# Kernel tuning notes

Hardware: AMD Instinct MI355X
Metric: run time of the kernel (lower is better)

The kernel has to match this reference:

```python
import jax, jax.numpy as jnp
import numpy as np

# dims: batch, seq_len, d_model, heads, head_dim, n_buckets
B, L, DM, H, DH, K = 4, 4096, 1024, 16, 64, 8
C = L // K            # chunk length after bucket sort (512); extra_len==0 for these dims
CS = 0.1              # cluster_score mixing weight


def setup_inputs() -> dict:
    key = jax.random.key(0)
    ks = jax.random.split(key, 12)
    s = 0.02
    def p(k, shape):
        return jax.random.normal(k, shape, jnp.float32) * s
    return {
        "inputs_q": jax.random.normal(ks[0], (B, L, DM), jnp.float32),
        "wq": p(ks[1], (DM, H, DH)), "bq": jnp.zeros((H, DH), jnp.float32),
        "wk": p(ks[2], (DM, H, DH)), "bk": jnp.zeros((H, DH), jnp.float32),
        "wv": p(ks[3], (DM, H, DH)), "bv": jnp.zeros((H, DH), jnp.float32),
        "w_shared": p(ks[4], (H, DH, K)),
        "w_qscore": p(ks[5], (H, DH, K)),
        "w_kscore": p(ks[6], (H, DH, K)),
        "wo": p(ks[7], (H, DH, DM)), "bo": jnp.zeros((DM,), jnp.float32),
    }


def reference(inputs_q, wq, bq, wk, bk, wv, bv, w_shared, w_qscore, w_kscore, wo, bo):
    scale = 1.0 / np.sqrt(DH)
    # QKV projections (DenseGeneral to (H, DH))
    q = jnp.einsum('bld,dhk->blhk', inputs_q, wq) + bq  # [B,L,H,DH]
    k = jnp.einsum('bld,dhk->blhk', inputs_q, wk) + bk
    v = jnp.einsum('bld,dhk->blhk', inputs_q, wv) + bv

    # learned linear cluster scores on stop-gradient q/k
    mix_q = (1.0 - CS) * w_shared + CS * w_qscore  # [H,DH,K]
    mix_k = (1.0 - CS) * w_shared + CS * w_kscore
    qs = jnp.einsum('blhd,hdk->blhk', jax.lax.stop_gradient(q), mix_q)  # [B,L,H,K]
    ksc = jnp.einsum('blhd,hdk->blhk', jax.lax.stop_gradient(k), mix_k)

    # bucket assignment = argmax learned score; per-(batch,head) stable sort by bucket id
    bq_id = jnp.argmax(qs, -1).transpose(0, 2, 1)   # [B,H,L]
    bk_id = jnp.argmax(ksc, -1).transpose(0, 2, 1)
    sort_q = jnp.argsort(bq_id, axis=-1)            # stable in jax
    sort_k = jnp.argsort(bk_id, axis=-1)

    qh = q.transpose(0, 2, 1, 3)  # [B,H,L,DH]
    kh = k.transpose(0, 2, 1, 3)
    vh = v.transpose(0, 2, 1, 3)
    sq = jnp.take_along_axis(qh, sort_q[..., None], axis=2).reshape(B, H, K, C, DH)
    sk = jnp.take_along_axis(kh, sort_k[..., None], axis=2).reshape(B, H, K, C, DH)
    sv = jnp.take_along_axis(vh, sort_k[..., None], axis=2).reshape(B, H, K, C, DH)

    # block attention within each bucket chunk
    logits = jnp.einsum('bhncd,bhned->bhnce', sq, sk) * scale  # [B,H,K,C,C]
    attn = jax.nn.softmax(logits, axis=-1)
    o = jnp.einsum('bhnce,bhned->bhncd', attn, sv).reshape(B, H, L, DH)

    # unsort back to original token order
    inv_q = jnp.argsort(sort_q, axis=-1)
    o = jnp.take_along_axis(o, inv_q[..., None], axis=2)  # [B,H,L,DH]
    o = o.transpose(0, 2, 1, 3)                            # [B,L,H,DH]

    out = jnp.einsum('blhd,hdo->blo', o, wo) + bo          # output projection

    # auxiliary load-balancing routing loss over buckets (extra_loss)
    p_q = jax.nn.softmax(qs, -1)
    p_k = jax.nn.softmax(ksc, -1)
    f_q = jax.nn.one_hot(jnp.argmax(qs, -1), K, dtype=qs.dtype)
    f_k = jax.nn.one_hot(jnp.argmax(ksc, -1), K, dtype=qs.dtype)
    lq = K * jnp.mean(jnp.sum(jnp.mean(f_q, 1) * jnp.mean(p_q, 1), -1))
    lk = K * jnp.mean(jnp.sum(jnp.mean(f_k, 1) * jnp.mean(p_k, 1), -1))
    extra_loss = 0.5 * (lq + lk)
    return out, extra_loss
```

## Files before the change

kernel.cpp:

```cpp
#include <hip/hip_runtime.h>
#include <hip/hip_bf16.h>

#define BB 4
#define LL 4096
#define DM 1024
#define HH 16
#define DHD 64
#define KB 8
#define BL 16384
#define FLAGCAP 131072

typedef __attribute__((ext_vector_type(8))) short short8;
typedef __attribute__((ext_vector_type(4))) short short4v;
typedef __attribute__((ext_vector_type(4))) float float4v;

#define MFMA16(A, Bx, C) __builtin_amdgcn_mfma_f32_16x16x32_bf16(A, Bx, C, 0, 0, 0)

static __device__ __forceinline__ short bf16s(float f) {
  __hip_bfloat16 h = __float2bfloat16(f);
  return *reinterpret_cast<short*>(&h);
}
static __device__ __forceinline__ float b2f(short s) {
  __hip_bfloat16 h = *reinterpret_cast<__hip_bfloat16*>(&s);
  return __bfloat162float(h);
}
static __device__ __forceinline__ void gl16(const void* g, void* l) {
  __builtin_amdgcn_global_load_lds(
      (const __attribute__((address_space(1))) void*)g,
      (__attribute__((address_space(3))) void*)l, 16, 0, 0);
}

__global__ __launch_bounds__(256) void xcvt(const float* __restrict__ x,
                                            __hip_bfloat16* __restrict__ xb) {
  int i = (blockIdx.x * 256 + threadIdx.x) * 8;
  float4 f0 = *reinterpret_cast<const float4*>(x + i);
  float4 f1 = *reinterpret_cast<const float4*>(x + i + 4);
  short8 o;
  o[0] = bf16s(f0.x); o[1] = bf16s(f0.y); o[2] = bf16s(f0.z); o[3] = bf16s(f0.w);
  o[4] = bf16s(f1.x); o[5] = bf16s(f1.y); o[6] = bf16s(f1.z); o[7] = bf16s(f1.w);
  *reinterpret_cast<short8*>(xb + i) = o;
}

__global__ __launch_bounds__(256) void prep_wt(const float* __restrict__ wq,
                                               const float* __restrict__ wk,
                                               const float* __restrict__ wv,
                                               const float* __restrict__ wo,
                                               __hip_bfloat16* __restrict__ wt_qkv,
                                               __hip_bfloat16* __restrict__ wt_o) {
  int blk = blockIdx.x;
  int s = blk >> 8;
  int rem = blk & 255;
  int k0 = (rem >> 4) * 64;
  int n0 = (rem & 15) * 64;
  const float* src = (s == 0) ? wq : (s == 1) ? wk : (s == 2) ? wv : wo;
  __hip_bfloat16* dst = (s < 3) ? (wt_qkv + (size_t)s * 1024 * 1024) : wt_o;
  __shared__ float ls[64][65];
  int t = threadIdx.x;
#pragma unroll
  for (int p = 0; p < 4; ++p) {
    int sid = p * 256 + t;
    int r = sid >> 4, c4 = sid & 15;
    float4 v = *reinterpret_cast<const float4*>(src + (size_t)(k0 + r) * 1024 + n0 + c4 * 4);
    ls[r][c4 * 4 + 0] = v.x; ls[r][c4 * 4 + 1] = v.y;
    ls[r][c4 * 4 + 2] = v.z; ls[r][c4 * 4 + 3] = v.w;
  }
  __syncthreads();
#pragma unroll
  for (int p = 0; p < 4; ++p) {
    int sid = p * 256 + t;
    int n = sid >> 4, kq = sid & 15;
    short4v pk;
#pragma unroll
    for (int j = 0; j < 4; ++j) pk[j] = bf16s(ls[kq * 4 + j][n]);
    *reinterpret_cast<short4v*>(dst + (size_t)(n0 + n) * 1024 + k0 + kq * 4) = pk;
  }
}

__global__ __launch_bounds__(256) void prep_wsc(const float* __restrict__ wq,
                                                const float* __restrict__ wk,
                                                const float* __restrict__ wsh,
                                                const float* __restrict__ wqs,
                                                const float* __restrict__ wks,
                                                const float* __restrict__ bq,
                                                const float* __restrict__ bk,
                                                double* __restrict__ wscg,
                                                double* __restrict__ bsc,
                                                __hip_bfloat16* __restrict__ whb,
                                                __hip_bfloat16* __restrict__ wmb) {
  int col = blockIdx.x;
  int side = col >> 7, h = (col >> 3) & 15, kk = col & 7;
  int g = side * 16 + h;
  const float* w = side ? wk : wq;
  const float* wscore = side ? wks : wqs;
  __shared__ double mix[64];
  int t = threadIdx.x;
  if (t < 64)
    mix[t] = 0.9 * (double)wsh[(h * 64 + t) * 8 + kk] +
             0.1 * (double)wscore[(h * 64 + t) * 8 + kk];
  __syncthreads();
#pragma unroll
  for (int p = 0; p < 4; ++p) {
    int d = p * 256 + t;
    double acc = 0.0;
    const float* wr = w + (size_t)d * 1024 + h * 64;
#pragma unroll
    for (int j = 0; j < 64; ++j) acc += (double)wr[j] * mix[j];
    wscg[((size_t)g * 1024 + d) * 8 + kk] = acc;
    short hi = bf16s((float)acc);
    short mid = bf16s((float)(acc - (double)b2f(hi)));
    *reinterpret_cast<short*>(whb + (size_t)col * 1024 + d) = hi;
    *reinterpret_cast<short*>(wmb + (size_t)col * 1024 + d) = mid;
  }
  if (t == 0) {
    const float* br = (side ? bk : bq) + h * 64;
    double acc = 0.0;
    for (int j = 0; j < 64; ++j) acc += (double)br[j] * mix[j];
    bsc[col] = acc;
  }
}

__global__ __launch_bounds__(256) void score_gemm(const float* __restrict__ x,
                                                  const __hip_bfloat16* __restrict__ whb,
                                                  const __hip_bfloat16* __restrict__ wmb,
                                                  const double* __restrict__ bsc,
                                                  float* __restrict__ S2) {
  __shared__ char sm[49152];
  int t = threadIdx.x;
  int m0 = blockIdx.x * 64;
  int n0 = blockIdx.y * 128;
  int lane = t & 63;
  int wu = __builtin_amdgcn_readfirstlane(t >> 6);
  int lm = lane & 15, quad = lane >> 4;
  int wmr = (wu & 1) * 32, wn = (wu >> 1) * 64;
  int rb = wu * 32, rr = lane >> 3, phys = lane & 7;
  float4v zero = {0.f, 0.f, 0.f, 0.f};
  float4v acc[2][4];
#pragma unroll
  for (int i = 0; i < 2; ++i)
#pragma unroll
    for (int j = 0; j < 4; ++j) acc[i][j] = zero;

  for (int k0 = 0; k0 < 1024; k0 += 64) {
    __syncthreads();
#pragma unroll
    for (int p = 0; p < 2; ++p) {
      int sid = p * 256 + t;
      int m = sid >> 3, kc = sid & 7;
      const float* ap = x + (size_t)(m0 + m) * 1024 + k0 + kc * 8;
      float4 f0 = *reinterpret_cast<const float4*>(ap);
      float4 f1 = *reinterpret_cast<const float4*>(ap + 4);
      float vv[8] = {f0.x, f0.y, f0.z, f0.w, f1.x, f1.y, f1.z, f1.w};
      short8 hi, lo;
#pragma unroll
      for (int e = 0; e < 8; ++e) {
        short h = bf16s(vv[e]);
        hi[e] = h;
        lo[e] = bf16s(vv[e] - b2f(h));
      }
      *reinterpret_cast<short8*>(sm + m * 128 + ((kc + m) & 7) * 16) = hi;
      *reinterpret_cast<short8*>(sm + 8192 + m * 128 + ((kc + m) & 7) * 16) = lo;
    }
#pragma unroll
    for (int p = 0; p < 4; ++p) {
      int row = rb + p * 8 + rr;
      int kc = (phys - row) & 7;
      gl16(whb + (size_t)(n0 + row) * 1024 + k0 + kc * 8, sm + 16384 + (rb + p * 8) * 128);
      gl16(wmb + (size_t)(n0 + row) * 1024 + k0 + kc * 8, sm + 32768 + (rb + p * 8) * 128);
    }
    __syncthreads();
#pragma unroll
    for (int kh = 0; kh < 2; ++kh) {
      short8 ah[2], al[2], bh[4], bm[4];
#pragma unroll
      for (int i = 0; i < 2; ++i) {
        int row = wmr + i * 16 + lm;
        int ph = ((kh * 4 + quad) + row) & 7;
        ah[i] = *reinterpret_cast<const short8*>(sm + row * 128 + ph * 16);
        al[i] = *reinterpret_cast<const short8*>(sm + 8192 + row * 128 + ph * 16);
      }
#pragma unroll
      for (int j = 0; j < 4; ++j) {
        int rn = wn + j * 16 + lm;
        int ph = ((kh * 4 + quad) + rn) & 7;
        bh[j] = *reinterpret_cast<const short8*>(sm + 16384 + rn * 128 + ph * 16);
        bm[j] = *reinterpret_cast<const short8*>(sm + 32768 + rn * 128 + ph * 16);
      }
#pragma unroll
      for (int i = 0; i < 2; ++i)
#pragma unroll
        for (int j = 0; j < 4; ++j) {
          acc[i][j] = MFMA16(ah[i], bh[j], acc[i][j]);
          acc[i][j] = MFMA16(ah[i], bm[j], acc[i][j]);
          acc[i][j] = MFMA16(al[i], bh[j], acc[i][j]);
        }
    }
  }

#pragma unroll
  for (int i = 0; i < 2; ++i)
#pragma unroll
    for (int j = 0; j < 4; ++j) {
      int n = n0 + wn + j * 16 + lm;
      float bias = (float)bsc[n];
#pragma unroll
      for (int r = 0; r < 4; ++r) {
        int row = m0 + wmr + i * 16 + quad * 4 + r;
        S2[(size_t)(n >> 3) * 131072 + row * 8 + (n & 7)] = acc[i][j][r] + bias;
      }
    }
}

__global__ __launch_bounds__(512) void bucket_kernel(const float* __restrict__ S2,
                                                     int* __restrict__ bid,
                                                     float* __restrict__ psumg,
                                                     int* __restrict__ flagcnt,
                                                     int* __restrict__ list) {
  int t = threadIdx.x;
  int lane = t & 63;
  int w = t >> 6;
  int T0 = blockIdx.x * 64;
  int tg = T0 + lane;
  int b = tg >> 12, l = tg & 4095;
#pragma unroll
  for (int gi = 0; gi < 4; ++gi) {
    int g = gi * 8 + w;
    const float* sp = S2 + (size_t)g * 131072 + tg * 8;
    float4 v0 = *reinterpret_cast<const float4*>(sp);
    float4 v1 = *reinterpret_cast<const float4*>(sp + 4);
    float v[8] = {v0.x, v0.y, v0.z, v0.w, v1.x, v1.y, v1.z, v1.w};
    float mx = v[0]; int am = 0;
#pragma unroll
    for (int j = 1; j < 8; ++j) { if (v[j] > mx) { mx = v[j]; am = j; } }
    float mx2 = -3.0e38f;
#pragma unroll
    for (int j = 0; j < 8; ++j) { if (j != am && v[j] > mx2) mx2 = v[j]; }
    int side = g >> 4, h = g & 15;
    int slab = (side * 4 + b) * 16 + h;
    bid[(slab << 12) | l] = am;
    if (mx - mx2 < 5e-4f) {
      int pos = atomicAdd(flagcnt, 1);
      if (pos < FLAGCAP) list[pos] = (slab << 12) | l;
    }
    float es = 0.f, e[8];
#pragma unroll
    for (int j = 0; j < 8; ++j) { e[j] = __expf(v[j] - mx); es += e[j]; }
    float inv = 1.f / es;
#pragma unroll
    for (int j = 0; j < 8; ++j) {
      float s = e[j] * inv;
      s += __shfl_xor(s, 1);  s += __shfl_xor(s, 2);  s += __shfl_xor(s, 4);
      s += __shfl_xor(s, 8);  s += __shfl_xor(s, 16); s += __shfl_xor(s, 32);
      if (lane == 0) atomicAdd(&psumg[slab * 8 + j], s);
    }
  }
}

__global__ __launch_bounds__(256) void refine_kernel(const float* __restrict__ x,
                                                     const double* __restrict__ wscg,
                                                     const double* __restrict__ bsc,
                                                     const int* __restrict__ flagcnt,
                                                     const int* __restrict__ list,
                                                     int* __restrict__ bid) {
  int lane = threadIdx.x & 63;
  int w = threadIdx.x >> 6;
  int cnt = flagcnt[0];
  if (cnt > FLAGCAP) cnt = FLAGCAP;
  for (int i = blockIdx.x * 4 + w; i < cnt; i += 1024) {
    int e = list[i];
    int slab = e >> 12, l = e & 4095;
    int side = slab >> 6, b = (slab >> 4) & 3, h = slab & 15;
    int g = side * 16 + h;
    int row = b * 4096 + l;
    double acc[8] = {0, 0, 0, 0, 0, 0, 0, 0};
    const float* xr = x + (size_t)row * 1024 + lane * 16;
    const double* wr = wscg + ((size_t)g * 1024 + lane * 16) * 8;
#pragma unroll
    for (int dd = 0; dd < 16; ++dd) {
      double xv = (double)xr[dd];
#pragma unroll
      for (int j = 0; j < 8; ++j) acc[j] += xv * wr[dd * 8 + j];
    }
#pragma unroll
    for (int j = 0; j < 8; ++j) {
      double v = acc[j];
      v += __shfl_xor(v, 32); v += __shfl_xor(v, 16); v += __shfl_xor(v, 8);
      v += __shfl_xor(v, 4);  v += __shfl_xor(v, 2);  v += __shfl_xor(v, 1);
      acc[j] = v + bsc[g * 8 + j];
    }
    if (lane == 0) {
      double mx = acc[0]; int am = 0;
#pragma unroll
      for (int j = 1; j < 8; ++j) { if (acc[j] > mx) { mx = acc[j]; am = j; } }
      bid[(slab << 12) | l] = am;
    }
  }
}

__global__ __launch_bounds__(256) void sort_kernel(const int* __restrict__ bid,
                                                   int* __restrict__ sortq,
                                                   int* __restrict__ sortk,
                                                   int* __restrict__ cntg) {
  int blk = blockIdx.x;
  int side = blk >> 6, b = (blk >> 4) & 3, h = blk & 15;
  const int* ids = bid + (((side * 4 + b) * 16 + h) << 12);
  int* outp = (side ? sortk : sortq) + ((b * 16 + h) << 12);
  __shared__ int cnt[8][257];
  __shared__ int base[8];
  int t = threadIdx.x;
  int loc[16];
  int hist[8] = {0, 0, 0, 0, 0, 0, 0, 0};
#pragma unroll
  for (int j = 0; j < 16; ++j) { loc[j] = ids[t * 16 + j] & 7; hist[loc[j]]++; }
#pragma unroll
  for (int k = 0; k < 8; ++k) cnt[k][t + 1] = hist[k];
  if (t < 8) cnt[t][0] = 0;
  __syncthreads();
  if (t < 8) {
    for (int i = 1; i <= 256; ++i) cnt[t][i] += cnt[t][i - 1];
  }
  __syncthreads();
  if (t == 0) {
    int run = 0;
    for (int k = 0; k < 8; ++k) { base[k] = run; run += cnt[k][256]; }
  }
  if (t < 8) cntg[((side * 4 + b) * 16 + h) * 8 + t] = cnt[t][256];
  __syncthreads();
#pragma unroll
  for (int j = 0; j < 16; ++j) {
    int k = loc[j];
    int before = 0;
#pragma unroll
    for (int i = 0; i < 16; ++i) before += (i < j && loc[i] == k) ? 1 : 0;
    int pos = base[k] + cnt[k][t] + before;
    outp[pos] = t * 16 + j;
  }
}

template <bool CBF16>
__global__ __launch_bounds__(512, 2) void gemm256(const __hip_bfloat16* __restrict__ A,
                                                  const __hip_bfloat16* __restrict__ Bt,
                                                  void* __restrict__ Cv,
                                                  const float* __restrict__ b0,
                                                  const float* __restrict__ b1,
                                                  const float* __restrict__ b2,
                                                  int nblk, int cpx) {
  __shared__ char sm[131072];
  int t = threadIdx.x;
  int blk = (blockIdx.x & 7) * cpx + (blockIdx.x >> 3);
  int m0 = (blk / nblk) * 256;
  int n0 = (blk % nblk) * 256;
  int lane = t & 63;
  int wu = __builtin_amdgcn_readfirstlane(t >> 6);
  int lm = lane & 15, quad = lane >> 4;
  int rr = lane >> 3, phys = lane & 7;
  int wrow = (wu & 1) * 64;
  int wcol = (wu >> 1) * 32;

  constexpr int QM[4] = {0, 0, 1, 1};
  constexpr int QN[4] = {0, 1, 1, 0};

  auto STAGE = [&](char* bufn, int j, int kS) {
    const int mat = (j == 1 || j == 2) ? 1 : 0;
    const int hm = (j >= 2) ? 1 : 0;
    const __hip_bfloat16* src = mat ? Bt : A;
    int gb = mat ? n0 : m0;
    char* lb = bufn + mat * 32768 + hm * 16384;
#pragma unroll
    for (int i = 0; i < 2; ++i) {
      int r = hm * 128 + (wu * 2 + i) * 8 + rr;
      int kc = (phys - r) & 7;
      gl16(src + (size_t)(gb + r) * 1024 + kS + kc * 8, lb + (wu * 2 + i) * 1024);
    }
  };

#pragma unroll
  for (int j = 0; j < 4; ++j) STAGE(sm, j, 0);

  float4v zero = {0.f, 0.f, 0.f, 0.f};
  float4v acc[4][4][2];
#pragma unroll
  for (int q = 0; q < 4; ++q)
#pragma unroll
    for (int mi = 0; mi < 4; ++mi)
#pragma unroll
      for (int ni = 0; ni < 2; ++ni) acc[q][mi][ni] = zero;

  short8 a[4][2], b[2][2];
  auto READA = [&](const char* bc, int qm) {
#pragma unroll
    for (int mi = 0; mi < 4; ++mi) {
      int row = qm * 128 + wrow + mi * 16 + lm;
#pragma unroll
      for (int ks = 0; ks < 2; ++ks) {
        int ph = ((ks * 4 + quad) + row) & 7;
        a[mi][ks] = *reinterpret_cast<const short8*>(bc + row * 128 + ph * 16);
      }
    }
  };
  auto READB = [&](const char* bc, int qn) {
#pragma unroll
    for (int ni = 0; ni < 2; ++ni) {
      int rn = qn * 128 + wcol + ni * 16 + lm;
#pragma unroll
      for (int ks = 0; ks < 2; ++ks) {
        int ph = ((ks * 4 + quad) + rn) & 7;
        b[ni][ks] = *reinterpret_cast<const short8*>(bc + 32768 + rn * 128 + ph * 16);
      }
    }
  };

#pragma unroll 1
  for (int kt = 0; kt < 16; ++kt) {
    char* bc = sm + ((kt & 1) << 16);
    char* bn = sm + (((kt & 1) ^ 1) << 16);
    int kS = (kt < 15) ? (kt + 1) * 64 : 960;
#pragma unroll
    for (int j = 0; j < 4; ++j) {
      if (j < 3) {
        asm volatile("s_waitcnt vmcnt(4)" ::: "memory");
        __builtin_amdgcn_s_barrier();
      }
      if (j == 0) { READA(bc, 0); READB(bc, 0); }
      else if (j == 1) { READB(bc, 1); }
      else if (j == 2) { READA(bc, 1); }
      else { READB(bc, 0); }
      STAGE(bn, j, kS);
      __builtin_amdgcn_s_setprio(1);
#pragma unroll
      for (int mi = 0; mi < 4; ++mi)
#pragma unroll
        for (int ni = 0; ni < 2; ++ni)
#pragma unroll
          for (int ks = 0; ks < 2; ++ks)
            acc[j][mi][ni] = MFMA16(a[mi][ks], b[ni][ks], acc[j][mi][ni]);
      __builtin_amdgcn_s_setprio(0);
    }
  }
  asm volatile("s_waitcnt vmcnt(0)" ::: "memory");

  if constexpr (CBF16) {
#pragma unroll
    for (int j = 0; j < 4; ++j)
#pragma unroll
      for (int mi = 0; mi < 4; ++mi)
#pragma unroll
        for (int ni = 0; ni < 2; ++ni) {
          int nn = n0 + QN[j] * 128 + wcol + ni * 16 + lm;
          int s = nn >> 10, nnb = nn & 1023;
          const float* bias = (s == 0) ? b0 : (s == 1) ? b1 : b2;
          float bvx = bias[nnb];
          __hip_bfloat16* C = (__hip_bfloat16*)Cv + (size_t)s * BL * 1024;
#pragma unroll
          for (int r = 0; r < 4; ++r) {
            int row = m0 + QM[j] * 128 + wrow + mi * 16 + quad * 4 + r;
            C[(size_t)row * 1024 + nnb] = __float2bfloat16(acc[j][mi][ni][r] + bvx);
          }
        }
  } else {
    float* C = (float*)Cv;
#pragma unroll
    for (int j = 0; j < 4; ++j)
#pragma unroll
      for (int mi = 0; mi < 4; ++mi)
#pragma unroll
        for (int ni = 0; ni < 2; ++ni) {
          int nn = n0 + QN[j] * 128 + wcol + ni * 16 + lm;
          float bvx = b0[nn];
#pragma unroll
          for (int r = 0; r < 4; ++r) {
            int row = m0 + QM[j] * 128 + wrow + mi * 16 + quad * 4 + r;
            C[(size_t)row * 1024 + nn] = acc[j][mi][ni][r] + bvx;
          }
        }
  }
}

__global__ __launch_bounds__(256) void vt_kernel(const __hip_bfloat16* __restrict__ vb,
                                                 const int* __restrict__ sortk,
                                                 __hip_bfloat16* __restrict__ vT) {
  int cid = blockIdx.x;
  int b = cid >> 7, h = (cid >> 3) & 15, n = cid & 7;
  int sbase = ((b * 16 + h) << 12) + n * 512;
  __shared__ __hip_bfloat16 ls[64][72];
  int t = threadIdx.x;
  for (int kt = 0; kt < 8; ++kt) {
    __syncthreads();
#pragma unroll
    for (int p = 0; p < 2; ++p) {
      int sid = p * 256 + t;
      int key = sid >> 3, kc = sid & 7;
      int tok = sortk[sbase + kt * 64 + key];
      short8 v = *reinterpret_cast<const short8*>(vb + ((size_t)(b * 4096 + tok) * 16 + h) * 64 + kc * 8);
      *reinterpret_cast<short8*>(&ls[key][kc * 8]) = v;
    }
    __syncthreads();
#pragma unroll
    for (int p = 0; p < 2; ++p) {
      int sid = p * 256 + t;
      int dim = sid >> 3, kc = sid & 7;
      short8 o;
#pragma unroll
      for (int j = 0; j < 8; ++j) o[j] = *reinterpret_cast<short*>(&ls[kc * 8 + j][dim]);
      *reinterpret_cast<short8*>(vT + ((size_t)cid * 64 + dim) * 512 + kt * 64 + kc * 8) = o;
    }
  }
}

__global__ __launch_bounds__(256) void attn_kernel(const __hip_bfloat16* __restrict__ qb,
                                                   const __hip_bfloat16* __restrict__ kb,
                                                   const __hip_bfloat16* __restrict__ vT,
                                                   const int* __restrict__ sortq,
                                                   const int* __restrict__ sortk,
                                                   __hip_bfloat16* __restrict__ ao) {
  __shared__ char sm[25600];
  int t = threadIdx.x;
  int lane = t & 63, w = t >> 6;
  int lm = lane & 15, quad = lane >> 4;
  int cid = blockIdx.x >> 3, qt = blockIdx.x & 7;
  int b = cid >> 7, h = (cid >> 3) & 15, n = cid & 7;
  int sbase = (b * 16 + h) << 12;
  int psOff = 16384 + w * 2304;

  int qtok = sortq[sbase + n * 512 + qt * 64 + w * 16 + lm];
  const __hip_bfloat16* qp = qb + ((size_t)(b * 4096 + qtok) * 16 + h) * 64 + quad * 8;
  short8 aq0 = *reinterpret_cast<const short8*>(qp);
  short8 aq1 = *reinterpret_cast<const short8*>(qp + 32);

  float4v zero = {0.f, 0.f, 0.f, 0.f};
  float4v accO[4];
#pragma unroll
  for (int i = 0; i < 4; ++i) accO[i] = zero;
  float lsum[4] = {0.f, 0.f, 0.f, 0.f};

  for (int kt = 0; kt < 8; ++kt) {
    __syncthreads();
#pragma unroll
    for (int p = 0; p < 2; ++p) {
      int sid = p * 256 + t;
      int row = sid >> 3, kc = sid & 7;
      int tok = sortk[sbase + n * 512 + kt * 64 + row];
      short8 kv = *reinterpret_cast<const short8*>(kb + ((size_t)(b * 4096 + tok) * 16 + h) * 64 + kc * 8);
      *reinterpret_cast<short8*>(sm + row * 128 + ((kc + row) & 7) * 16) = kv;
      short8 vv = *reinterpret_cast<const short8*>(vT + ((size_t)cid * 64 + row) * 512 + kt * 64 + kc * 8);
      *reinterpret_cast<short8*>(sm + 8192 + row * 128 + ((kc + row) & 7) * 16) = vv;
    }
    __syncthreads();
#pragma unroll
    for (int nt = 0; nt < 4; ++nt) {
      int key = nt * 16 + lm;
      int ph0 = (quad + key) & 7;
      int ph1 = (4 + quad + key) & 7;
      short8 bk0 = *reinterpret_cast<const short8*>(sm + key * 128 + ph0 * 16);
      short8 bk1 = *reinterpret_cast<const short8*>(sm + key * 128 + ph1 * 16);
      float4v S = zero;
      S = MFMA16(aq0, bk0, S);
      S = MFMA16(aq1, bk1, S);
#pragma unroll
      for (int r = 0; r < 4; ++r) {
        float e = __expf(S[r] * 0.125f);
        lsum[r] += e;
        *reinterpret_cast<short*>(sm + psOff + (quad * 4 + r) * 144 + key * 2) = bf16s(e);
      }
    }
    __builtin_amdgcn_s_waitcnt(0);
#pragma unroll
    for (int ks = 0; ks < 2; ++ks) {
      short8 ap = *reinterpret_cast<const short8*>(sm + psOff + lm * 144 + ks * 64 + quad * 16);
#pragma unroll
      for (int dt = 0; dt < 4; ++dt) {
        int dim = dt * 16 + lm;
        int ph = (ks * 4 + quad + dim) & 7;
        short8 bv = *reinterpret_cast<const short8*>(sm + 8192 + dim * 128 + ph * 16);
        accO[dt] = MFMA16(ap, bv, accO[dt]);
      }
    }
  }
#pragma unroll
  for (int r = 0; r < 4; ++r) {
    float l = lsum[r];
    l += __shfl_xor(l, 1); l += __shfl_xor(l, 2);
    l += __shfl_xor(l, 4); l += __shfl_xor(l, 8);
    lsum[r] = 1.f / l;
  }
#pragma unroll
  for (int dt = 0; dt < 4; ++dt)
#pragma unroll
    for (int r = 0; r < 4; ++r)
      *reinterpret_cast<short*>(sm + psOff + (quad * 4 + r) * 144 + (dt * 16 + lm) * 2) =
          bf16s(accO[dt][r] * lsum[r]);
  __builtin_amdgcn_s_waitcnt(0);
  int q2 = lane >> 2, c = lane & 3;
  int tok2 = sortq[sbase + n * 512 + qt * 64 + w * 16 + q2];
  __hip_bfloat16* op = ao + ((size_t)(b * 4096 + tok2) * 16 + h) * 64;
  short8 o0 = *reinterpret_cast<const short8*>(sm + psOff + q2 * 144 + c * 16);
  short8 o1 = *reinterpret_cast<const short8*>(sm + psOff + q2 * 144 + (c + 4) * 16);
  *reinterpret_cast<short8*>(op + c * 8) = o0;
  *reinterpret_cast<short8*>(op + (c + 4) * 8) = o1;
}

__global__ __launch_bounds__(1024) void loss_kernel(const int* __restrict__ cntg,
                                                    const float* __restrict__ psumg,
                                                    float* __restrict__ out) {
  int t = threadIdx.x;
  float term = ((float)cntg[t] * (1.f / 4096.f)) * (psumg[t] * (1.f / 4096.f));
#pragma unroll
  for (int o = 1; o < 64; o <<= 1) term += __shfl_xor(term, o);
  __shared__ float wsum[16];
  if ((t & 63) == 0) wsum[t >> 6] = term;
  __syncthreads();
  if (t == 0) {
    float s = 0.f;
    for (int i = 0; i < 16; ++i) s += wsum[i];
    out[16777216] = s * (1.f / 16.f);
  }
}

extern "C" void kernel_launch(void* const* d_in, const int* in_sizes, int n_in,
                              void* d_out, int out_size, void* d_ws, size_t ws_size,
                              hipStream_t stream) {
  (void)in_sizes; (void)n_in; (void)out_size; (void)ws_size;
  const float* x   = (const float*)d_in[0];
  const float* wq  = (const float*)d_in[1];
  const float* bq  = (const float*)d_in[2];
  const float* wk  = (const float*)d_in[3];
  const float* bk  = (const float*)d_in[4];
  const float* wv  = (const float*)d_in[5];
  const float* bv  = (const float*)d_in[6];
  const float* wsh = (const float*)d_in[7];
  const float* wqs = (const float*)d_in[8];
  const float* wks = (const float*)d_in[9];
  const float* wo  = (const float*)d_in[10];
  const float* bo  = (const float*)d_in[11];

  char* ws = (char*)d_ws;
  __hip_bfloat16* wt_qkv = (__hip_bfloat16*)(ws + 0);
  __hip_bfloat16* wt_o   = (__hip_bfloat16*)(ws + 6291456);
  double* wscg  = (double*)(ws + 8388608);
  double* bsc   = (double*)(ws + 10485760);
  __hip_bfloat16* qkv  = (__hip_bfloat16*)(ws + 10487808);
  __hip_bfloat16* whb = (__hip_bfloat16*)(ws + 109051904);
  __hip_bfloat16* wmb = (__hip_bfloat16*)(ws + 109576192);
  int* flagcnt = (int*)(ws + 110100480);
  int* list    = (int*)(ws + 110100736);
  __hip_bfloat16* attn = (__hip_bfloat16*)(ws + 111151104);
  float* S2 = (float*)(ws + 111151104);
  int* bid    = (int*)(ws + 144705536);
  int* sortq  = (int*)(ws + 146802688);
  int* sortk  = (int*)(ws + 147851264);
  float* psumg = (float*)(ws + 148899840);
  int* cntg    = (int*)(ws + 148903936);
  __hip_bfloat16* vT = (__hip_bfloat16*)d_out;
  __hip_bfloat16* xb = (__hip_bfloat16*)((char*)d_out + 33554432);
  float* out = (float*)d_out;

  hipMemsetAsync(psumg, 0, 8192, stream);
  hipMemsetAsync(flagcnt, 0, 4, stream);
  prep_wt<<<1024, 256, 0, stream>>>(wq, wk, wv, wo, wt_qkv, wt_o);
  prep_wsc<<<256, 256, 0, stream>>>(wq, wk, wsh, wqs, wks, bq, bk, wscg, bsc, whb, wmb);
  xcvt<<<8192, 256, 0, stream>>>(x, xb);
  score_gemm<<<dim3(256, 2), 256, 0, stream>>>(x, whb, wmb, bsc, S2);
  bucket_kernel<<<256, 512, 0, stream>>>(S2, bid, psumg, flagcnt, list);
  refine_kernel<<<256, 256, 0, stream>>>(x, wscg, bsc, flagcnt, list, bid);
  sort_kernel<<<128, 256, 0, stream>>>(bid, sortq, sortk, cntg);
  gemm256<true><<<768, 512, 0, stream>>>(xb, wt_qkv, qkv, bq, bk, bv, 12, 96);
  vt_kernel<<<512, 256, 0, stream>>>(qkv + (size_t)2 * BL * 1024, sortk, vT);
  attn_kernel<<<4096, 256, 0, stream>>>(qkv, qkv + (size_t)BL * 1024, vT, sortq, sortk, attn);
  gemm256<false><<<256, 512, 0, stream>>>(attn, wt_o, (void*)out, bo, bo, bo, 4, 32);
  loss_kernel<<<1, 1024, 0, stream>>>(cntg, psumg, out);
}
```

Baseline: 530.3 us.

## Fuse bf16 input conversion and bucket argmax/softmax into score GEMM epilogue

The separate xcvt kernel is removed: the score GEMM already splits x into bf16 hi/lo, and its y==0 blocks now also write the hi part to xb. The S2 score buffer and bucket_kernel are eliminated. Argmax, second-max flagging, softmax and the per-bucket probability sums are computed in the GEMM epilogue with lane shuffles across the 8 bucket columns. This saves two launches, a full pass over x and the S2 round trip through memory, at the cost of extra global stores and atomics inside the GEMM.

After: 538.3 us. About the same (+1.5%).

```diff
diff --git a/kernel.cpp b/kernel.cpp
--- a/kernel.cpp
+++ b/kernel.cpp
@@ -28,17 +28,6 @@
   __builtin_amdgcn_global_load_lds(
       (const __attribute__((address_space(1))) void*)g,
       (__attribute__((address_space(3))) void*)l, 16, 0, 0);
-}
-
-__global__ __launch_bounds__(256) void xcvt(const float* __restrict__ x,
-                                            __hip_bfloat16* __restrict__ xb) {
-  int i = (blockIdx.x * 256 + threadIdx.x) * 8;
-  float4 f0 = *reinterpret_cast<const float4*>(x + i);
-  float4 f1 = *reinterpret_cast<const float4*>(x + i + 4);
-  short8 o;
-  o[0] = bf16s(f0.x); o[1] = bf16s(f0.y); o[2] = bf16s(f0.z); o[3] = bf16s(f0.w);
-  o[4] = bf16s(f1.x); o[5] = bf16s(f1.y); o[6] = bf16s(f1.z); o[7] = bf16s(f1.w);
-  *reinterpret_cast<short8*>(xb + i) = o;
 }
 
 __global__ __launch_bounds__(256) void prep_wt(const float* __restrict__ wq,
@@ -123,7 +112,11 @@
                                                   const __hip_bfloat16* __restrict__ whb,
                                                   const __hip_bfloat16* __restrict__ wmb,
                                                   const double* __restrict__ bsc,
-                                                  float* __restrict__ S2) {
+                                                  __hip_bfloat16* __restrict__ xb,
+                                                  int* __restrict__ bid,
+                                                  float* __restrict__ psumg,
+                                                  int* __restrict__ flagcnt,
+                                                  int* __restrict__ list) {
   __shared__ char sm[49152];
   int t = threadIdx.x;
   int m0 = blockIdx.x * 64;
@@ -159,6 +152,8 @@
       }
       *reinterpret_cast<short8*>(sm + m * 128 + ((kc + m) & 7) * 16) = hi;
       *reinterpret_cast<short8*>(sm + 8192 + m * 128 + ((kc + m) & 7) * 16) = lo;
+      if (blockIdx.y == 0)
+        *reinterpret_cast<short8*>(xb + (size_t)(m0 + m) * 1024 + k0 + kc * 8) = hi;
     }
 #pragma unroll
     for (int p = 0; p < 4; ++p) {
@@ -196,62 +191,49 @@
     }
   }
 
-#pragma unroll
-  for (int i = 0; i < 2; ++i)
-#pragma unroll
-    for (int j = 0; j < 4; ++j) {
-      int n = n0 + wn + j * 16 + lm;
-      float bias = (float)bsc[n];
-#pragma unroll
-      for (int r = 0; r < 4; ++r) {
-        int row = m0 + wmr + i * 16 + quad * 4 + r;
-        S2[(size_t)(n >> 3) * 131072 + row * 8 + (n & 7)] = acc[i][j][r] + bias;
-      }
-    }
-}
-
-__global__ __launch_bounds__(512) void bucket_kernel(const float* __restrict__ S2,
-                                                     int* __restrict__ bid,
-                                                     float* __restrict__ psumg,
-                                                     int* __restrict__ flagcnt,
-                                                     int* __restrict__ list) {
-  int t = threadIdx.x;
-  int lane = t & 63;
-  int w = t >> 6;
-  int T0 = blockIdx.x * 64;
-  int tg = T0 + lane;
-  int b = tg >> 12, l = tg & 4095;
-#pragma unroll
-  for (int gi = 0; gi < 4; ++gi) {
-    int g = gi * 8 + w;
-    const float* sp = S2 + (size_t)g * 131072 + tg * 8;
-    float4 v0 = *reinterpret_cast<const float4*>(sp);
-    float4 v1 = *reinterpret_cast<const float4*>(sp + 4);
-    float v[8] = {v0.x, v0.y, v0.z, v0.w, v1.x, v1.y, v1.z, v1.w};
-    float mx = v[0]; int am = 0;
-#pragma unroll
-    for (int j = 1; j < 8; ++j) { if (v[j] > mx) { mx = v[j]; am = j; } }
-    float mx2 = -3.0e38f;
-#pragma unroll
-    for (int j = 0; j < 8; ++j) { if (j != am && v[j] > mx2) mx2 = v[j]; }
+  int b = m0 >> 12;
+  int l0 = m0 & 4095;
+  int kk = lm & 7;
+#pragma unroll
+  for (int j = 0; j < 4; ++j) {
+    int n = n0 + wn + j * 16 + lm;
+    int g = n >> 3;
     int side = g >> 4, h = g & 15;
     int slab = (side * 4 + b) * 16 + h;
-    bid[(slab << 12) | l] = am;
-    if (mx - mx2 < 5e-4f) {
-      int pos = atomicAdd(flagcnt, 1);
-      if (pos < FLAGCAP) list[pos] = (slab << 12) | l;
-    }
-    float es = 0.f, e[8];
-#pragma unroll
-    for (int j = 0; j < 8; ++j) { e[j] = __expf(v[j] - mx); es += e[j]; }
-    float inv = 1.f / es;
-#pragma unroll
-    for (int j = 0; j < 8; ++j) {
-      float s = e[j] * inv;
-      s += __shfl_xor(s, 1);  s += __shfl_xor(s, 2);  s += __shfl_xor(s, 4);
-      s += __shfl_xor(s, 8);  s += __shfl_xor(s, 16); s += __shfl_xor(s, 32);
-      if (lane == 0) atomicAdd(&psumg[slab * 8 + j], s);
-    }
+    float bias = (float)bsc[n];
+    float pp = 0.f;
+#pragma unroll
+    for (int i = 0; i < 2; ++i)
+#pragma unroll
+      for (int r = 0; r < 4; ++r) {
+        float v = acc[i][j][r] + bias;
+        float bmx = v; int bi = kk;
+#pragma unroll
+        for (int o = 1; o < 8; o <<= 1) {
+          float vo = __shfl_xor(bmx, o);
+          int io = __shfl_xor(bi, o);
+          if (vo > bmx || (vo == bmx && io < bi)) { bmx = vo; bi = io; }
+        }
+        float vm = (kk == bi) ? -3.0e38f : v;
+#pragma unroll
+        for (int o = 1; o < 8; o <<= 1) vm = fmaxf(vm, __shfl_xor(vm, o));
+        float e = __expf(v - bmx);
+        float es = e;
+#pragma unroll
+        for (int o = 1; o < 8; o <<= 1) es += __shfl_xor(es, o);
+        pp += e * (1.f / es);
+        int l = l0 + wmr + i * 16 + quad * 4 + r;
+        if (kk == 0) {
+          bid[(slab << 12) | l] = bi;
+          if (bmx - vm < 5e-4f) {
+            int pos = atomicAdd(flagcnt, 1);
+            if (pos < FLAGCAP) list[pos] = (slab << 12) | l;
+          }
+        }
+      }
+    pp += __shfl_xor(pp, 16);
+    pp += __shfl_xor(pp, 32);
+    if (quad == 0) atomicAdd(&psumg[slab * 8 + kk], pp);
   }
 }
 
@@ -643,7 +625,6 @@
   int* flagcnt = (int*)(ws + 110100480);
   int* list    = (int*)(ws + 110100736);
   __hip_bfloat16* attn = (__hip_bfloat16*)(ws + 111151104);
-  float* S2 = (float*)(ws + 111151104);
   int* bid    = (int*)(ws + 144705536);
   int* sortq  = (int*)(ws + 146802688);
   int* sortk  = (int*)(ws + 147851264);
@@ -657,9 +638,7 @@
   hipMemsetAsync(flagcnt, 0, 4, stream);
   prep_wt<<<1024, 256, 0, stream>>>(wq, wk, wv, wo, wt_qkv, wt_o);
   prep_wsc<<<256, 256, 0, stream>>>(wq, wk, wsh, wqs, wks, bq, bk, wscg, bsc, whb, wmb);
-  xcvt<<<8192, 256, 0, stream>>>(x, xb);
-  score_gemm<<<dim3(256, 2), 256, 0, stream>>>(x, whb, wmb, bsc, S2);
-  bucket_kernel<<<256, 512, 0, stream>>>(S2, bid, psumg, flagcnt, list);
+  score_gemm<<<dim3(256, 2), 256, 0, stream>>>(x, whb, wmb, bsc, xb, bid, psumg, flagcnt, list);
   refine_kernel<<<256, 256, 0, stream>>>(x, wscg, bsc, flagcnt, list, bid);
   sort_kernel<<<128, 256, 0, stream>>>(bid, sortq, sortk, cntg);
   gemm256<true><<<768, 512, 0, stream>>>(xb, wt_qkv, qkv, bq, bk, bv, 12, 96);
```
